# Kernel optimization log

Measured on AMD Instinct MI355X. Metric: run time of the kernel, lower is better.

Reference implementation:

```python
import jax, jax.numpy as jnp
import numpy as np
import math

L = 6          # num_layers
D = 512        # hidden_dim
S = 2048       # seq_len
B = 8          # batch
ODIM = 1       # output_dim
SCALES = (24.0, 720.0)


def setup_inputs() -> dict:
    key = jax.random.key(0)
    ks = jax.random.split(key, 12)
    def n(k, shape, scale=0.02):
        return jax.random.normal(k, shape, dtype=jnp.float32) * scale
    return {
        "z": jax.random.normal(ks[0], (B, S, 1), dtype=jnp.float32),
        "c": jax.random.normal(ks[1], (B, S, 1), dtype=jnp.float32),
        "enc_w": n(ks[2], (D, 2)), "enc_b": jnp.zeros((D,), jnp.float32),
        "beta": jnp.ones((L, len(SCALES)), jnp.float32),
        "wq": n(ks[3], (L, D, D)), "bq": jnp.zeros((L, D), jnp.float32),
        "wk": n(ks[4], (L, D, D)), "bk": jnp.zeros((L, D), jnp.float32),
        "wv": n(ks[5], (L, D, D)), "bv": jnp.zeros((L, D), jnp.float32),
        "ln1_w": jnp.ones((L, D), jnp.float32), "ln1_b": jnp.zeros((L, D), jnp.float32),
        "ln2_w": jnp.ones((L, D), jnp.float32), "ln2_b": jnp.zeros((L, D), jnp.float32),
        "ff1_w": n(ks[6], (L, 4 * D, D)), "ff1_b": jnp.zeros((L, 4 * D), jnp.float32),
        "ff2_w": n(ks[7], (L, D, 4 * D)), "ff2_b": jnp.zeros((L, D), jnp.float32),
        "out_w": n(ks[8], (ODIM, D)), "out_b": jnp.zeros((ODIM,), jnp.float32),
    }


def _ln(x, w, b, eps=1e-5):
    m = jnp.mean(x, axis=-1, keepdims=True)
    v = jnp.var(x, axis=-1, keepdims=True)
    return (x - m) * jax.lax.rsqrt(v + eps) * w + b


def _posenc(seq_len, dim):
    pos = jnp.arange(seq_len, dtype=jnp.float32)[:, None]
    div = jnp.exp(jnp.arange(0, dim, 2, dtype=jnp.float32) * (-(math.log(10000.0) / dim)))
    pe = jnp.zeros((seq_len, dim), jnp.float32)
    pe = pe.at[:, 0::2].set(jnp.sin(pos * div))
    pe = pe.at[:, 1::2].set(jnp.cos(pos * div))
    return pe


def reference(z, c, enc_w, enc_b, beta, wq, bq, wk, bk, wv, bv,
              ln1_w, ln1_b, ln2_w, ln2_b, ff1_w, ff1_b, ff2_w, ff2_b,
              out_w, out_b):
    # SequenceEncoder: cat(z,c) -> Linear(2, D) -> + sinusoidal PE
    x = jnp.concatenate([z, c], axis=-1) @ enc_w.T + enc_b       # [B,S,D]
    seq_len, d = x.shape[1], x.shape[2]
    x = x + _posenc(seq_len, d)[None]
    sqrt_d = math.sqrt(d)

    idx = jnp.arange(seq_len, dtype=jnp.float32)
    dist = jnp.abs(idx[:, None] - idx[None, :])                  # [S,S]

    for l in range(L):
        # pre-norm with ln1 (applied twice in the original code - replicated)
        xn = _ln(x, ln1_w[l], ln1_b[l])
        Q = xn @ wq[l].T + bq[l]
        K = xn @ wk[l].T + bk[l]
        V = xn @ wv[l].T + bv[l]
        attn = jnp.einsum('bid,bjd->bij', Q, K) / sqrt_d          # [B,S,S]
        bias = beta[l, 0] * jnp.cos(2.0 * math.pi * dist / SCALES[0]) \
             + beta[l, 1] * jnp.cos(2.0 * math.pi * dist / SCALES[1])
        probs = jax.nn.softmax(attn + bias, axis=-1)
        att_out = jnp.einsum('bij,bjd->bid', probs, V)
        # original applies layer_norm_1 again to the residual sum
        x = _ln(x + att_out, ln1_w[l], ln1_b[l])
        xn2 = _ln(x, ln2_w[l], ln2_b[l])
        h = jax.nn.relu(xn2 @ ff1_w[l].T + ff1_b[l])
        x = x + h @ ff2_w[l].T + ff2_b[l]

    return x @ out_w.T + out_b                                    # [B,S,ODIM]
```

## Files before the change

kernel.cpp:

```cpp
#include <hip/hip_runtime.h>
#include <hip/hip_fp8.h>
#include <math.h>

#define BB 8
#define SS 2048
#define DD 512
#define LL 6
#define FFD 2048

typedef _Float16 half_t;
typedef __attribute__((ext_vector_type(8))) _Float16 half8;
typedef __attribute__((ext_vector_type(4))) float f32x4;

enum { EPI_NONE = 0, EPI_RELU = 2, EPI_RES = 3, EPI_ATTN = 4, EPI_QKV = 5, EPI_PV = 6 };

__device__ __forceinline__ unsigned char f2e4m3(float v) {
    __hip_fp8_e4m3 f(v);
    return f.__x;
}
__device__ __forceinline__ float e4m3_2f(unsigned char b) {
    __hip_fp8_e4m3 f; f.__x = b;
    return (float)f;
}

__device__ __forceinline__ void gl_lds16(const void* g, void* l) {
    __builtin_amdgcn_global_load_lds(
        (const __attribute__((address_space(1))) unsigned int*)g,
        (__attribute__((address_space(3))) unsigned int*)l,
        16, 0, 0);
}

__device__ __forceinline__ void blockReduce2(float& a, float& b, float* sm) {
#pragma unroll
    for (int off = 32; off; off >>= 1) {
        a += __shfl_down(a, off);
        b += __shfl_down(b, off);
    }
    int lane = threadIdx.x & 63;
    int w = threadIdx.x >> 6;
    if (lane == 0) { sm[w] = a; sm[4 + w] = b; }
    __syncthreads();
    a = sm[0] + sm[1] + sm[2] + sm[3];
    b = sm[4] + sm[5] + sm[6] + sm[7];
    __syncthreads();
}

__global__ __launch_bounds__(256) void encode_kernel(
    const float* __restrict__ z, const float* __restrict__ c,
    const float* __restrict__ enc_w, const float* __restrict__ enc_b,
    float* __restrict__ x)
{
    int idx = blockIdx.x * 256 + threadIdx.x;
    int d  = idx & (DD - 1);
    int bs = idx >> 9;
    int s  = bs & (SS - 1);
    float v = z[bs] * enc_w[2 * d] + c[bs] * enc_w[2 * d + 1] + enc_b[d];
    float div = expf(-(float)(d & ~1) * (9.210340371976184f / 512.0f));
    float ang = (float)s * div;
    v += (d & 1) ? cosf(ang) : sinf(ang);
    x[idx] = v;
}

__global__ __launch_bounds__(256) void convert_layer_kernel(
    const float* __restrict__ wq, const float* __restrict__ wk,
    const float* __restrict__ wv, const float* __restrict__ f1,
    const float* __restrict__ f2, half_t* __restrict__ wqkv,
    half_t* __restrict__ f1h, half_t* __restrict__ f2h)
{
    const int NQ = DD * DD;
    int i = blockIdx.x * 256 + threadIdx.x;
    if (i < 3 * NQ) {
        int which = i >> 18, j = i & (NQ - 1);
        const float* s = (which == 0) ? wq : (which == 1) ? wk : wv;
        wqkv[i] = (half_t)s[j];
    } else {
        int k = i - 3 * NQ;
        if (k < FFD * DD) f1h[k] = (half_t)f1[k];
        else              f2h[k - FFD * DD] = (half_t)f2[k - FFD * DD];
    }
}

__global__ __launch_bounds__(256) void bias_table_kernel(
    const float* __restrict__ beta, float* __restrict__ tbl)
{
    int i = blockIdx.x * 256 + threadIdx.x;
    int l = i >> 11, d = i & (SS - 1);
    tbl[i] = beta[2 * l] * cosf(0.2617993877991494f * d)
           + beta[2 * l + 1] * cosf(0.008726646259971648f * d);
}

__global__ __launch_bounds__(256) void ln_kernel(
    const float* __restrict__ src, const float* __restrict__ w,
    const float* __restrict__ b, half_t* __restrict__ dst)
{
    __shared__ float sm[8];
    size_t row = blockIdx.x;
    const float* p = src + row * DD;
    int t = threadIdx.x;
    float v0 = p[t], v1 = p[t + 256];
    float s = v0 + v1, sq = v0 * v0 + v1 * v1;
    blockReduce2(s, sq, sm);
    float mean = s * (1.0f / DD);
    float var  = sq * (1.0f / DD) - mean * mean;
    float rs   = rsqrtf(var + 1e-5f);
    dst[row * DD + t]       = (half_t)((v0 - mean) * rs * w[t] + b[t]);
    dst[row * DD + t + 256] = (half_t)((v1 - mean) * rs * w[t + 256] + b[t + 256]);
}

__global__ __launch_bounds__(256) void ln_ln_kernel(
    float* __restrict__ x,
    const float* __restrict__ w1, const float* __restrict__ b1,
    const float* __restrict__ w2, const float* __restrict__ b2,
    half_t* __restrict__ xn)
{
    __shared__ float sm[8];
    size_t row = blockIdx.x;
    int t = threadIdx.x;
    float v0 = x[row * DD + t];
    float v1 = x[row * DD + t + 256];
    float s = v0 + v1, sq = v0 * v0 + v1 * v1;
    blockReduce2(s, sq, sm);
    float mean = s * (1.0f / DD);
    float var  = sq * (1.0f / DD) - mean * mean;
    float rs   = rsqrtf(var + 1e-5f);
    float y0 = (v0 - mean) * rs * w1[t] + b1[t];
    float y1 = (v1 - mean) * rs * w1[t + 256] + b1[t + 256];
    x[row * DD + t]       = y0;
    x[row * DD + t + 256] = y1;
    s = y0 + y1; sq = y0 * y0 + y1 * y1;
    blockReduce2(s, sq, sm);
    mean = s * (1.0f / DD);
    var  = sq * (1.0f / DD) - mean * mean;
    rs   = rsqrtf(var + 1e-5f);
    xn[row * DD + t]       = (half_t)((y0 - mean) * rs * w2[t] + b2[t]);
    xn[row * DD + t + 256] = (half_t)((y1 - mean) * rs * w2[t + 256] + b2[t + 256]);
}

template<typename TIN, int MT, int EPI, int SWZ = 0>
__global__ __launch_bounds__(256) void gemm_mfma(
    const void* __restrict__ Ap, const void* __restrict__ Wp,
    const float* __restrict__ bias, void* __restrict__ Cp,
    int N, int K, float alpha,
    long long sA, long long sW, long long sC,
    const float* __restrict__ biasK, const float* __restrict__ biasV,
    unsigned char* __restrict__ Ck, unsigned char* __restrict__ Cv)
{
    constexpr int TM = MT / 32;
    constexpr int ES = (int)sizeof(TIN);
    constexpr int ABYTES = MT * 32 * ES;
    constexpr int BBYTES = 128 * 32 * ES;
    __shared__ __align__(16) unsigned char As[2 * ABYTES];
    __shared__ __align__(16) unsigned char Bs[2 * BBYTES];

    int bxi, byi, bzi;
    if (SWZ == 1) {
        const int id = blockIdx.x;
        const int cc = id & 7, rr = id >> 3;
        bxi = rr & 15;
        const int ss = cc + 8 * (rr >> 4);
        byi = ss & 15; bzi = ss >> 4;
    } else { bxi = blockIdx.x; byi = blockIdx.y; bzi = blockIdx.z; }

    const int z = bzi;
    const unsigned char* A = (const unsigned char*)Ap + (size_t)z * sA * ES;
    const unsigned char* W = (const unsigned char*)Wp + (size_t)z * sW * ES;
    float*  Cf = (float*)Cp  + (size_t)z * sC;
    half_t* Ch = (half_t*)Cp + (size_t)z * sC;
    unsigned char* C8 = (unsigned char*)Cp + (size_t)z * sC;

    const int tid = threadIdx.x;
    const int wv = tid >> 6, ln = tid & 63;
    const int bm = bxi * MT, bn = byi * 128;
    const int wm = (wv & 1) * (MT / 2), wn = (wv >> 1) * 64;

    const int srow  = (ES == 2) ? (wv * 16 + (ln >> 2)) : (wv * 32 + (ln >> 1));
    const int scolB = (ES == 2) ? ((ln & 3) * 16) : ((ln & 1) * 16);
    const unsigned char* Ag = A + (size_t)(bm + srow) * K * ES + scolB;
    const unsigned char* Bg = W + (size_t)(bn + srow) * K * ES + scolB;

    f32x4 acc[TM][4] = {};
    float rs[TM];
#pragma unroll
    for (int i = 0; i < TM; ++i) rs[i] = 0.f;

    const int lane15 = ln & 15, quad = ln >> 4;
    const int nIter = K >> 5;

    {
        unsigned char* la = As + wv * 1024;
        unsigned char* lb = Bs + wv * 1024;
        if (ES == 2) {
            gl_lds16(Ag, la);
            if (MT == 128) gl_lds16(Ag + (size_t)64 * K * ES, la + 4096);
            gl_lds16(Bg, lb);
            gl_lds16(Bg + (size_t)64 * K * ES, lb + 4096);
        } else {
            if (MT == 128 || wv < 2) gl_lds16(Ag, la);
            gl_lds16(Bg, lb);
        }
    }
    __syncthreads();

    for (int it = 0; it < nIter; ++it) {
        const int cur = it & 1;
        if (it + 1 < nIter) {
            const size_t ko = (size_t)(it + 1) * 32 * ES;
            unsigned char* la = As + (cur ^ 1) * ABYTES + wv * 1024;
            unsigned char* lb = Bs + (cur ^ 1) * BBYTES + wv * 1024;
            if (ES == 2) {
                gl_lds16(Ag + ko, la);
                if (MT == 128) gl_lds16(Ag + (size_t)64 * K * ES + ko, la + 4096);
                gl_lds16(Bg + ko, lb);
                gl_lds16(Bg + (size_t)64 * K * ES + ko, lb + 4096);
            } else {
                if (MT == 128 || wv < 2) gl_lds16(Ag + ko, la);
                gl_lds16(Bg + ko, lb);
            }
        }

        const unsigned char* Ab = As + cur * ABYTES;
        const unsigned char* Bb = Bs + cur * BBYTES;
        half8 aF[TM], bF[4];
        long aF8[TM], bF8[4];
#pragma unroll
        for (int i = 0; i < TM; ++i) {
            if constexpr (ES == 2)
                aF[i] = *(const half8*)(Ab + ((wm + i * 16 + lane15) * 32 + quad * 8) * 2);
            else
                aF8[i] = *(const long*)(Ab + (wm + i * 16 + lane15) * 32 + quad * 8);
        }
#pragma unroll
        for (int j = 0; j < 4; ++j) {
            if constexpr (ES == 2)
                bF[j] = *(const half8*)(Bb + ((wn + j * 16 + lane15) * 32 + quad * 8) * 2);
            else
                bF8[j] = *(const long*)(Bb + (wn + j * 16 + lane15) * 32 + quad * 8);
        }

        if (EPI == EPI_PV) {
#pragma unroll
            for (int i = 0; i < TM; ++i) {
                union { long l; unsigned char b[8]; } u; u.l = aF8[i];
#pragma unroll
                for (int e = 0; e < 8; ++e) rs[i] += e4m3_2f(u.b[e]);
            }
        }

#pragma unroll
        for (int i = 0; i < TM; ++i)
#pragma unroll
            for (int j = 0; j < 4; ++j) {
                if constexpr (ES == 2)
                    acc[i][j] = __builtin_amdgcn_mfma_f32_16x16x32_f16(
                        aF[i], bF[j], acc[i][j], 0, 0, 0);
                else
                    acc[i][j] = __builtin_amdgcn_mfma_f32_16x16x32_fp8_fp8(
                        aF8[i], bF8[j], acc[i][j], 0, 0, 0);
            }

        __syncthreads();
    }

    float inv[TM][4];
    if (EPI == EPI_PV) {
#pragma unroll
        for (int i = 0; i < TM; ++i) {
            rs[i] += __shfl_xor(rs[i], 16);
            rs[i] += __shfl_xor(rs[i], 32);
            rs[i] = 1.0f / rs[i];
#pragma unroll
            for (int r = 0; r < 4; ++r)
                inv[i][r] = __shfl(rs[i], quad * 4 + r);
        }
    }

#pragma unroll
    for (int i = 0; i < TM; ++i) {
        const int m0 = bm + wm + i * 16 + quad * 4;
#pragma unroll
        for (int j = 0; j < 4; ++j) {
            const int gn = bn + wn + j * 16 + lane15;
            if (EPI == EPI_QKV) {
                const int seg = gn >> 9, nn = gn & (DD - 1);
                if (seg == 2) {
                    unsigned int pk = 0;
#pragma unroll
                    for (int r = 0; r < 4; ++r)
                        pk |= (unsigned int)f2e4m3(acc[i][j][r] + biasV[nn]) << (8 * r);
                    const int b = m0 >> 11, s0 = m0 & (SS - 1);
                    *(unsigned int*)&Cv[((size_t)b * DD + nn) * SS + s0] = pk;
                } else {
                    const float bs = (seg == 0) ? bias[nn] : biasK[nn];
                    unsigned char* dst = (seg == 0) ? C8 : Ck;
#pragma unroll
                    for (int r = 0; r < 4; ++r)
                        dst[(size_t)(m0 + r) * DD + nn] = f2e4m3(acc[i][j][r] + bs);
                }
            } else {
#pragma unroll
                for (int r = 0; r < 4; ++r) {
                    const int gm = m0 + r;
                    float v = acc[i][j][r];
                    if (EPI == EPI_ATTN) {
                        int dist = gm - gn; if (dist < 0) dist = -dist;
                        v = __expf(fminf(v * alpha + bias[dist], 6.0f));
                        C8[(size_t)gm * N + gn] = f2e4m3(v);
                    } else if (EPI == EPI_PV) {
                        const size_t idx = (size_t)gm * N + gn;
                        Cf[idx] = v * inv[i][r] + Cf[idx];
                    } else if (EPI == EPI_RELU) {
                        Ch[(size_t)gm * N + gn] = (half_t)fmaxf(v + bias[gn], 0.0f);
                    } else {
                        const size_t idx = (size_t)gm * N + gn;
                        Cf[idx] = v + bias[gn] + Cf[idx];
                    }
                }
            }
        }
    }
}

__global__ __launch_bounds__(256) void out_kernel(
    const float* __restrict__ x, const float* __restrict__ ow,
    const float* __restrict__ ob, float* __restrict__ out)
{
    int row = blockIdx.x * 4 + (threadIdx.x >> 6);
    int lane = threadIdx.x & 63;
    const float* p = x + (size_t)row * DD;
    float s = 0.f;
#pragma unroll
    for (int k = 0; k < 8; ++k) s += p[lane + 64 * k] * ow[lane + 64 * k];
#pragma unroll
    for (int off = 32; off; off >>= 1) s += __shfl_down(s, off);
    if (lane == 0) out[row] = s + ob[0];
}

extern "C" void kernel_launch(void* const* d_in, const int* in_sizes, int n_in,
                              void* d_out, int out_size, void* d_ws, size_t ws_size,
                              hipStream_t stream)
{
    (void)in_sizes; (void)n_in; (void)out_size; (void)ws_size;
    const float* z     = (const float*)d_in[0];
    const float* c     = (const float*)d_in[1];
    const float* enc_w = (const float*)d_in[2];
    const float* enc_b = (const float*)d_in[3];
    const float* beta  = (const float*)d_in[4];
    const float* wq    = (const float*)d_in[5];
    const float* bq    = (const float*)d_in[6];
    const float* wk    = (const float*)d_in[7];
    const float* bk    = (const float*)d_in[8];
    const float* wv    = (const float*)d_in[9];
    const float* bv    = (const float*)d_in[10];
    const float* ln1w  = (const float*)d_in[11];
    const float* ln1b  = (const float*)d_in[12];
    const float* ln2w  = (const float*)d_in[13];
    const float* ln2b  = (const float*)d_in[14];
    const float* ff1w  = (const float*)d_in[15];
    const float* ff1b  = (const float*)d_in[16];
    const float* ff2w  = (const float*)d_in[17];
    const float* ff2b  = (const float*)d_in[18];
    const float* ow    = (const float*)d_in[19];
    const float* ob    = (const float*)d_in[20];

    const size_t BSD = (size_t)BB * SS * DD;
    const size_t BSS = (size_t)BB * SS * SS;

    char* p = (char*)d_ws;
    float*  x    = (float*)p;  p += BSD * 4;
    half_t* xnh  = (half_t*)p; p += BSD * 2;
    unsigned char* sch = (unsigned char*)p; p += BSS;
    unsigned char* qh  = (unsigned char*)p; p += BSD;
    unsigned char* kh  = (unsigned char*)p; p += BSD;
    unsigned char* vth = (unsigned char*)p; p += BSD;
    half_t* hh   = (half_t*)p; p += (size_t)BB * SS * FFD * 2;
    half_t* wqkv = (half_t*)p; p += (size_t)3 * DD * DD * 2;
    half_t* f1h  = (half_t*)p; p += (size_t)FFD * DD * 2;
    half_t* f2h  = (half_t*)p; p += (size_t)FFD * DD * 2;
    float*  tbl  = (float*)p;

    const float alpha = 0.044194173824159216f;
    const int BS = BB * SS;
    const long long sQ = (long long)SS * DD, sP = (long long)SS * SS,
                    sV = (long long)DD * SS;
    const int CONV_BLKS = (3 * DD * DD + 2 * FFD * DD) / 256;

    bias_table_kernel<<<LL * SS / 256, 256, 0, stream>>>(beta, tbl);
    encode_kernel<<<BS * DD / 256, 256, 0, stream>>>(z, c, enc_w, enc_b, x);

    for (int l = 0; l < LL; ++l) {
        convert_layer_kernel<<<CONV_BLKS, 256, 0, stream>>>(
            wq + (size_t)l * DD * DD, wk + (size_t)l * DD * DD,
            wv + (size_t)l * DD * DD, ff1w + (size_t)l * FFD * DD,
            ff2w + (size_t)l * DD * FFD, wqkv, f1h, f2h);

        ln_kernel<<<BS, 256, 0, stream>>>(x, ln1w + l * DD, ln1b + l * DD, xnh);

        gemm_mfma<half_t, 128, EPI_QKV><<<dim3(BS / 128, 12, 1), 256, 0, stream>>>(
            xnh, wqkv, bq + l * DD, qh, 1536, DD, 0, 0, 0, 0,
            bk + l * DD, bv + l * DD, kh, vth);

        gemm_mfma<unsigned char, 128, EPI_ATTN, 1><<<dim3(2048, 1, 1), 256, 0, stream>>>(
            qh, kh, tbl + l * SS, sch, SS, DD, alpha, sQ, sQ, sP,
            nullptr, nullptr, nullptr, nullptr);

        gemm_mfma<unsigned char, 64, EPI_PV><<<dim3(SS / 64, DD / 128, BB), 256, 0, stream>>>(
            sch, vth, nullptr, x, DD, SS, 0, sP, sV, sQ,
            nullptr, nullptr, nullptr, nullptr);

        ln_ln_kernel<<<BS, 256, 0, stream>>>(x, ln1w + l * DD, ln1b + l * DD,
                                             ln2w + l * DD, ln2b + l * DD, xnh);

        gemm_mfma<half_t, 128, EPI_RELU><<<dim3(BS / 128, FFD / 128, 1), 256, 0, stream>>>(
            xnh, f1h, ff1b + l * FFD, hh, FFD, DD, 0, 0, 0, 0,
            nullptr, nullptr, nullptr, nullptr);
        gemm_mfma<half_t, 64, EPI_RES><<<dim3(BS / 64, DD / 128, 1), 256, 0, stream>>>(
            hh, f2h, ff2b + l * DD, x, DD, FFD, 0, 0, 0, 0,
            nullptr, nullptr, nullptr, nullptr);
    }

    out_kernel<<<BS / 4, 256, 0, stream>>>(x, ow, ob, (float*)d_out);
}
```

Before: 2.018 ms.

## Double fp8 GEMM K-tile to 64 and compute PV row sums via MFMA

For fp8 GEMMs the K step per iteration is doubled to 64, so each stage loads a full 64-byte row per tile. This halves the loop iterations and barriers and unifies the load path with the fp16 path. The softmax denominator in the PV epilogue is now produced by an extra MFMA against a vector of fp8 ones instead of per-element fp8-to-float conversions and cross-lane shuffles. This removes scalar conversion work from the inner loop, at the cost of one extra MFMA per row tile and per sub-step.

New measurement: 2.340 ms. +15.9%, slower.

```diff
diff --git a/kernel.cpp b/kernel.cpp
--- a/kernel.cpp
+++ b/kernel.cpp
@@ -17,10 +17,6 @@
 __device__ __forceinline__ unsigned char f2e4m3(float v) {
     __hip_fp8_e4m3 f(v);
     return f.__x;
-}
-__device__ __forceinline__ float e4m3_2f(unsigned char b) {
-    __hip_fp8_e4m3 f; f.__x = b;
-    return (float)f;
 }
 
 __device__ __forceinline__ void gl_lds16(const void* g, void* l) {
@@ -147,8 +143,10 @@
 {
     constexpr int TM = MT / 32;
     constexpr int ES = (int)sizeof(TIN);
-    constexpr int ABYTES = MT * 32 * ES;
-    constexpr int BBYTES = 128 * 32 * ES;
+    constexpr int BK = (ES == 2) ? 32 : 64;
+    constexpr int NS = (ES == 2) ? 1 : 2;
+    constexpr int ABYTES = MT * 64;
+    constexpr int BBYTES = 128 * 64;
     __shared__ __align__(16) unsigned char As[2 * ABYTES];
     __shared__ __align__(16) unsigned char Bs[2 * BBYTES];
 
@@ -173,105 +171,92 @@
     const int bm = bxi * MT, bn = byi * 128;
     const int wm = (wv & 1) * (MT / 2), wn = (wv >> 1) * 64;
 
-    const int srow  = (ES == 2) ? (wv * 16 + (ln >> 2)) : (wv * 32 + (ln >> 1));
-    const int scolB = (ES == 2) ? ((ln & 3) * 16) : ((ln & 1) * 16);
+    const int srow  = wv * 16 + (ln >> 2);
+    const int scolB = (ln & 3) * 16;
     const unsigned char* Ag = A + (size_t)(bm + srow) * K * ES + scolB;
     const unsigned char* Bg = W + (size_t)(bn + srow) * K * ES + scolB;
 
     f32x4 acc[TM][4] = {};
-    float rs[TM];
-#pragma unroll
-    for (int i = 0; i < TM; ++i) rs[i] = 0.f;
+    f32x4 accd[TM] = {};
+    const long ONES8 = 0x3838383838383838L;
 
     const int lane15 = ln & 15, quad = ln >> 4;
-    const int nIter = K >> 5;
+    const int nIter = K / BK;
 
     {
         unsigned char* la = As + wv * 1024;
         unsigned char* lb = Bs + wv * 1024;
-        if (ES == 2) {
-            gl_lds16(Ag, la);
-            if (MT == 128) gl_lds16(Ag + (size_t)64 * K * ES, la + 4096);
-            gl_lds16(Bg, lb);
-            gl_lds16(Bg + (size_t)64 * K * ES, lb + 4096);
-        } else {
-            if (MT == 128 || wv < 2) gl_lds16(Ag, la);
-            gl_lds16(Bg, lb);
-        }
+        gl_lds16(Ag, la);
+        if (MT == 128) gl_lds16(Ag + (size_t)64 * K * ES, la + 4096);
+        gl_lds16(Bg, lb);
+        gl_lds16(Bg + (size_t)64 * K * ES, lb + 4096);
     }
     __syncthreads();
 
     for (int it = 0; it < nIter; ++it) {
         const int cur = it & 1;
         if (it + 1 < nIter) {
-            const size_t ko = (size_t)(it + 1) * 32 * ES;
+            const size_t ko = (size_t)(it + 1) * 64;
             unsigned char* la = As + (cur ^ 1) * ABYTES + wv * 1024;
             unsigned char* lb = Bs + (cur ^ 1) * BBYTES + wv * 1024;
-            if (ES == 2) {
-                gl_lds16(Ag + ko, la);
-                if (MT == 128) gl_lds16(Ag + (size_t)64 * K * ES + ko, la + 4096);
-                gl_lds16(Bg + ko, lb);
-                gl_lds16(Bg + (size_t)64 * K * ES + ko, lb + 4096);
-            } else {
-                if (MT == 128 || wv < 2) gl_lds16(Ag + ko, la);
-                gl_lds16(Bg + ko, lb);
-            }
+            gl_lds16(Ag + ko, la);
+            if (MT == 128) gl_lds16(Ag + (size_t)64 * K * ES + ko, la + 4096);
+            gl_lds16(Bg + ko, lb);
+            gl_lds16(Bg + (size_t)64 * K * ES + ko, lb + 4096);
         }
 
         const unsigned char* Ab = As + cur * ABYTES;
         const unsigned char* Bb = Bs + cur * BBYTES;
-        half8 aF[TM], bF[4];
-        long aF8[TM], bF8[4];
-#pragma unroll
-        for (int i = 0; i < TM; ++i) {
-            if constexpr (ES == 2)
-                aF[i] = *(const half8*)(Ab + ((wm + i * 16 + lane15) * 32 + quad * 8) * 2);
-            else
-                aF8[i] = *(const long*)(Ab + (wm + i * 16 + lane15) * 32 + quad * 8);
-        }
-#pragma unroll
-        for (int j = 0; j < 4; ++j) {
-            if constexpr (ES == 2)
-                bF[j] = *(const half8*)(Bb + ((wn + j * 16 + lane15) * 32 + quad * 8) * 2);
-            else
-                bF8[j] = *(const long*)(Bb + (wn + j * 16 + lane15) * 32 + quad * 8);
-        }
-
-        if (EPI == EPI_PV) {
-#pragma unroll
-            for (int i = 0; i < TM; ++i) {
-                union { long l; unsigned char b[8]; } u; u.l = aF8[i];
-#pragma unroll
-                for (int e = 0; e < 8; ++e) rs[i] += e4m3_2f(u.b[e]);
-            }
-        }
-
-#pragma unroll
-        for (int i = 0; i < TM; ++i)
-#pragma unroll
-            for (int j = 0; j < 4; ++j) {
-                if constexpr (ES == 2)
+
+        if constexpr (ES == 2) {
+            half8 aF[TM], bF[4];
+#pragma unroll
+            for (int i = 0; i < TM; ++i)
+                aF[i] = *(const half8*)(Ab + (wm + i * 16 + lane15) * 64 + quad * 16);
+#pragma unroll
+            for (int j = 0; j < 4; ++j)
+                bF[j] = *(const half8*)(Bb + (wn + j * 16 + lane15) * 64 + quad * 16);
+#pragma unroll
+            for (int i = 0; i < TM; ++i)
+#pragma unroll
+                for (int j = 0; j < 4; ++j)
                     acc[i][j] = __builtin_amdgcn_mfma_f32_16x16x32_f16(
                         aF[i], bF[j], acc[i][j], 0, 0, 0);
-                else
-                    acc[i][j] = __builtin_amdgcn_mfma_f32_16x16x32_fp8_fp8(
-                        aF8[i], bF8[j], acc[i][j], 0, 0, 0);
+        } else {
+            long aF8[TM][NS], bF8[4][NS];
+#pragma unroll
+            for (int s = 0; s < NS; ++s) {
+#pragma unroll
+                for (int i = 0; i < TM; ++i)
+                    aF8[i][s] = *(const long*)(Ab + (wm + i * 16 + lane15) * 64 + s * 32 + quad * 8);
+#pragma unroll
+                for (int j = 0; j < 4; ++j)
+                    bF8[j][s] = *(const long*)(Bb + (wn + j * 16 + lane15) * 64 + s * 32 + quad * 8);
             }
+#pragma unroll
+            for (int s = 0; s < NS; ++s)
+#pragma unroll
+                for (int i = 0; i < TM; ++i) {
+#pragma unroll
+                    for (int j = 0; j < 4; ++j)
+                        acc[i][j] = __builtin_amdgcn_mfma_f32_16x16x32_fp8_fp8(
+                            aF8[i][s], bF8[j][s], acc[i][j], 0, 0, 0);
+                    if (EPI == EPI_PV)
+                        accd[i] = __builtin_amdgcn_mfma_f32_16x16x32_fp8_fp8(
+                            aF8[i][s], ONES8, accd[i], 0, 0, 0);
+                }
+        }
 
         __syncthreads();
     }
 
-    float inv[TM][4];
+    float invd[TM][4];
     if (EPI == EPI_PV) {
 #pragma unroll
-        for (int i = 0; i < TM; ++i) {
-            rs[i] += __shfl_xor(rs[i], 16);
-            rs[i] += __shfl_xor(rs[i], 32);
-            rs[i] = 1.0f / rs[i];
+        for (int i = 0; i < TM; ++i)
 #pragma unroll
             for (int r = 0; r < 4; ++r)
-                inv[i][r] = __shfl(rs[i], quad * 4 + r);
-        }
+                invd[i][r] = 1.0f / accd[i][r];
     }
 
 #pragma unroll
@@ -307,7 +292,7 @@
                         C8[(size_t)gm * N + gn] = f2e4m3(v);
                     } else if (EPI == EPI_PV) {
                         const size_t idx = (size_t)gm * N + gn;
-                        Cf[idx] = v * inv[i][r] + Cf[idx];
+                        Cf[idx] = v * invd[i][r] + Cf[idx];
                     } else if (EPI == EPI_RELU) {
                         Ch[(size_t)gm * N + gn] = (half_t)fmaxf(v + bias[gn], 0.0f);
                     } else {
```
